# Kernel tuning notes

Hardware: AMD Instinct MI355X
Metric: run time of the kernel (lower is better)

The kernel has to match this reference:

```python
import jax, jax.numpy as jnp
import numpy as np

T, B, N = 1000, 64, 512
DT = 0.01
EL, VR, TR, TINF = -0.07, -0.07, -0.06, -0.05
A_VAL = 2.6239240169525146
A1_VAL = -0.015625353902578354
A2_VAL = -1.0590057373046875
B_VAL = 12.77495288848877
G_VAL = 45.24007797241211
K1, K2 = 200.0, 20.0
R1, R2 = 0.3858567178249359, -1.1421641111373901
C = 1.0


def setup_inputs() -> dict:
    key = jax.random.key(0)
    x = jax.random.normal(key, (T, B, N), dtype=jnp.float32)
    linear = jnp.ones((1, N), jnp.float32)
    a = jnp.full((1, N), A_VAL, jnp.float32)
    A1 = jnp.full((1, N), A1_VAL * C, jnp.float32)
    A2 = jnp.full((1, N), A2_VAL * C, jnp.float32)
    return {"x": x, "linear": linear, "a": a, "A1": A1, "A2": A2}


def _spike(v):
    # Heaviside step (forward of SurrGradSpike)
    return (v > 0).astype(v.dtype)


def reference(x, linear, a, A1, A2):
    G = G_VAL * C

    def step(state, xt):
        V, i1, i2, Thr = state
        i1 = i1 - K1 * i1 * DT
        i2 = i2 - K2 * i2 * DT
        V = V + DT * (linear * xt + i1 + i2 - G * (V - EL)) / C
        Thr = Thr + DT * (a * (V - EL) - B_VAL * (Thr - TINF))
        spk = _spike(V - Thr)
        i1 = (1.0 - spk) * i1 + spk * (R1 * i1 + A1)
        i2 = (1.0 - spk) * i2 + spk * (R2 * i2 + A2)
        Thr = (1.0 - spk) * Thr + spk * jnp.maximum(Thr, TR)
        V = (1.0 - spk) * V + spk * VR
        return (V, i1, i2, Thr), spk

    Bd, Nd = x.shape[1], x.shape[2]
    init = (
        jnp.full((Bd, Nd), EL, x.dtype),   # V
        jnp.zeros((Bd, Nd), x.dtype),      # i1
        jnp.zeros((Bd, Nd), x.dtype),      # i2
        jnp.full((Bd, Nd), TINF, x.dtype), # Thr
    )
    _, spikes = jax.lax.scan(step, init, x)
    return spikes  # [T, B, N] (original returns np.array of per-step spikes)
```

## Files before the change

### kernel.cpp

```cpp
#include <hip/hip_runtime.h>


#define T_STEPS 1000
#define B_DIM 64
#define N_DIM 512
#define BN (B_DIM * N_DIM)

#define K_CHUNK 20
#define NCHUNK (T_STEPS / K_CHUNK)

#define C_DT   0.01f
#define C_EL   (-0.07f)
#define C_VR   (-0.07f)
#define C_TR   (-0.06f)
#define C_TINF (-0.05f)
#define C_B    12.77495288848877f
#define C_G    45.24007797241211f
#define C_K1   200.0f
#define C_K2   20.0f
#define C_R1   0.3858567178249359f
#define C_R2   (-1.1421641111373901f)

typedef const __attribute__((address_space(1))) void* gp_t;
typedef __attribute__((address_space(3))) void* lp_t;

__device__ __forceinline__ float mn_step(float xt, float lin, float av,
                                         float A1v, float A2v,
                                         float& V, float& i1, float& i2,
                                         float& Thr)
{
#pragma clang fp contract(off)
    i1 = i1 - (C_K1 * i1) * C_DT;
    i2 = i2 - (C_K2 * i2) * C_DT;
    float p  = lin * xt;
    float q  = p + i1;
    float r  = q + i2;
    float e  = V - C_EL;
    float g  = C_G * e;
    float s  = r - g;
    float d  = C_DT * s;
    V = V + d;
    float e2 = V - C_EL;
    float u  = av * e2;
    float w  = Thr - C_TINF;
    float bw = C_B * w;
    float s2 = u - bw;
    float d2 = C_DT * s2;
    Thr = Thr + d2;
    float diff = V - Thr;
    bool  sb   = diff > 0.0f;
    float spk  = sb ? 1.0f : 0.0f;
    float i1r = (C_R1 * i1) + A1v;
    float i2r = (C_R2 * i2) + A2v;
    i1  = sb ? i1r : i1;
    i2  = sb ? i2r : i2;
    float tm = fmaxf(Thr, C_TR);
    Thr = sb ? tm : Thr;
    V   = sb ? C_VR : V;
    return spk;
}

__global__ __launch_bounds__(128) void mn_neuron_kernel(
    const float* __restrict__ x, const float* __restrict__ linear,
    const float* __restrict__ a, const float* __restrict__ A1,
    const float* __restrict__ A2, float* __restrict__ out)
{
#pragma clang fp contract(off)
    __shared__ float lds[2][K_CHUNK][64];

    const int lane = threadIdx.x & 63;
    const int wid  = threadIdx.x >> 6;
    const int blk  = blockIdx.x;

    if (wid == 1) {
        const float* pl = x + (size_t)(lane >> 4) * BN
                            + (size_t)blk * 64 + (size_t)(lane & 15) * 4;

        {
#pragma unroll
            for (int s = 0; s < K_CHUNK / 4; ++s) {
                __builtin_amdgcn_global_load_lds(
                    (gp_t)(pl + (size_t)(s * 4) * BN),
                    (lp_t)&lds[0][s * 4][0], 16, 0, 0);
            }
            __builtin_amdgcn_s_waitcnt(0x0F70);
        }
        __syncthreads();

        for (int c = 0; c < NCHUNK; ++c) {
            if (c + 1 < NCHUNK) {
                const float* pc = pl + (size_t)((c + 1) * K_CHUNK) * BN;
                float* dst = &lds[(c + 1) & 1][0][0];
#pragma unroll
                for (int s = 0; s < K_CHUNK / 4; ++s) {
                    __builtin_amdgcn_global_load_lds(
                        (gp_t)(pc + (size_t)(s * 4) * BN),
                        (lp_t)(dst + s * 4 * 64), 16, 0, 0);
                }
                __builtin_amdgcn_s_waitcnt(0x0F70);
            }
            __syncthreads();
        }
    } else {
        const int idx = blk * 64 + lane;
        const int n   = idx & (N_DIM - 1);

        const float lin = linear[n];
        const float av  = a[n];
        const float A1v = A1[n];
        const float A2v = A2[n];

        float V   = C_EL;
        float i1  = 0.0f;
        float i2  = 0.0f;
        float Thr = C_TINF;

        float* op = out + idx;

        __syncthreads();

        for (int c = 0; c < NCHUNK; ++c) {
            const float* src = &lds[c & 1][0][lane];

            float xv[K_CHUNK];
#pragma unroll
            for (int j = 0; j < K_CHUNK; ++j)
                xv[j] = src[j * 64];

            __builtin_amdgcn_sched_barrier(0);

#pragma unroll
            for (int j = 0; j < K_CHUNK; ++j) {
                float spk = mn_step(xv[j], lin, av, A1v, A2v, V, i1, i2, Thr);
                *op = spk;
                op += BN;
            }
            __syncthreads();
        }
    }
}

extern "C" void kernel_launch(void* const* d_in, const int* in_sizes, int n_in,
                              void* d_out, int out_size, void* d_ws, size_t ws_size,
                              hipStream_t stream) {
    const float* x      = (const float*)d_in[0];
    const float* linear = (const float*)d_in[1];
    const float* a      = (const float*)d_in[2];
    const float* A1     = (const float*)d_in[3];
    const float* A2     = (const float*)d_in[4];
    float* out = (float*)d_out;

    mn_neuron_kernel<<<BN / 64, 128, 0, stream>>>(x, linear, a, A1, A2, out);
}
```

Baseline: 237.0 us.

## Move compute-wave barrier before compute and use nontemporal spike stores

The compute wave now loads its whole LDS chunk into registers with inline ds_read asm and waits for completion. It then hits the barrier immediately, instead of after running the 20 timesteps, so the loader wave can refill the buffer while compute proceeds. __syncthreads is replaced with raw s_barrier, and spike outputs are written with nontemporal stores to reduce cache pollution. The risk is that the inline asm and raw barriers bypass compiler fences, so correctness depends on the explicit waitcnt ordering.

```diff
diff --git a/kernel.cpp b/kernel.cpp
--- a/kernel.cpp
+++ b/kernel.cpp
@@ -23,6 +23,7 @@
 
 typedef const __attribute__((address_space(1))) void* gp_t;
 typedef __attribute__((address_space(3))) void* lp_t;
+typedef __attribute__((address_space(3))) float* lpf_t;
 
 __device__ __forceinline__ float mn_step(float xt, float lin, float av,
                                          float A1v, float A2v,
@@ -85,7 +86,7 @@
             }
             __builtin_amdgcn_s_waitcnt(0x0F70);
         }
-        __syncthreads();
+        __builtin_amdgcn_s_barrier();
 
         for (int c = 0; c < NCHUNK; ++c) {
             if (c + 1 < NCHUNK) {
@@ -99,7 +100,7 @@
                 }
                 __builtin_amdgcn_s_waitcnt(0x0F70);
             }
-            __syncthreads();
+            __builtin_amdgcn_s_barrier();
         }
     } else {
         const int idx = blk * 64 + lane;
@@ -117,25 +118,49 @@
 
         float* op = out + idx;
 
-        __syncthreads();
+        __builtin_amdgcn_s_barrier();
 
         for (int c = 0; c < NCHUNK; ++c) {
-            const float* src = &lds[c & 1][0][lane];
+            lpf_t lptr = (lpf_t)&lds[c & 1][0][lane];
 
             float xv[K_CHUNK];
-#pragma unroll
-            for (int j = 0; j < K_CHUNK; ++j)
-                xv[j] = src[j * 64];
+            asm volatile(
+                "ds_read_b32 %0,  %20 offset:0\n\t"
+                "ds_read_b32 %1,  %20 offset:256\n\t"
+                "ds_read_b32 %2,  %20 offset:512\n\t"
+                "ds_read_b32 %3,  %20 offset:768\n\t"
+                "ds_read_b32 %4,  %20 offset:1024\n\t"
+                "ds_read_b32 %5,  %20 offset:1280\n\t"
+                "ds_read_b32 %6,  %20 offset:1536\n\t"
+                "ds_read_b32 %7,  %20 offset:1792\n\t"
+                "ds_read_b32 %8,  %20 offset:2048\n\t"
+                "ds_read_b32 %9,  %20 offset:2304\n\t"
+                "ds_read_b32 %10, %20 offset:2560\n\t"
+                "ds_read_b32 %11, %20 offset:2816\n\t"
+                "ds_read_b32 %12, %20 offset:3072\n\t"
+                "ds_read_b32 %13, %20 offset:3328\n\t"
+                "ds_read_b32 %14, %20 offset:3584\n\t"
+                "ds_read_b32 %15, %20 offset:3840\n\t"
+                "ds_read_b32 %16, %20 offset:4096\n\t"
+                "ds_read_b32 %17, %20 offset:4352\n\t"
+                "ds_read_b32 %18, %20 offset:4608\n\t"
+                "ds_read_b32 %19, %20 offset:4864\n\t"
+                "s_waitcnt lgkmcnt(0)"
+                : "=&v"(xv[0]),  "=&v"(xv[1]),  "=&v"(xv[2]),  "=&v"(xv[3]),
+                  "=&v"(xv[4]),  "=&v"(xv[5]),  "=&v"(xv[6]),  "=&v"(xv[7]),
+                  "=&v"(xv[8]),  "=&v"(xv[9]),  "=&v"(xv[10]), "=&v"(xv[11]),
+                  "=&v"(xv[12]), "=&v"(xv[13]), "=&v"(xv[14]), "=&v"(xv[15]),
+                  "=&v"(xv[16]), "=&v"(xv[17]), "=&v"(xv[18]), "=&v"(xv[19])
+                : "v"(lptr));
 
-            __builtin_amdgcn_sched_barrier(0);
+            __builtin_amdgcn_s_barrier();
 
 #pragma unroll
             for (int j = 0; j < K_CHUNK; ++j) {
                 float spk = mn_step(xv[j], lin, av, A1v, A2v, V, i1, i2, Thr);
-                *op = spk;
+                __builtin_nontemporal_store(spk, op);
                 op += BN;
             }
-            __syncthreads();
         }
     }
 }
```

After: 240.5 us. About the same (+1.5%).
